# Optimization experiments

Hardware: AMD Instinct MI355X
Metric: run time of the kernel (lower is better)

The kernel has to match this reference:

```python
import jax, jax.numpy as jnp
import numpy as np

D, H, L, V, B, S, M, MAXLEN = 512, 8, 6, 32000, 16, 128, 196, 256
DK = D // H


def layernorm(x, g, b, eps):
    mu = jnp.mean(x, axis=-1, keepdims=True)
    var = jnp.mean((x - mu) ** 2, axis=-1, keepdims=True)
    return (x - mu) / jnp.sqrt(var + eps) * g + b


def mha(q_in, k_in, v_in, qw, qb, kw, kb, vw, vb, ow, ob, lng, lnb, mask):
    bs, sq = q_in.shape[0], q_in.shape[1]
    sk = k_in.shape[1]
    residual = q_in
    q = (q_in @ qw + qb).reshape(bs, sq, H, DK).transpose(0, 2, 1, 3)
    k = (k_in @ kw + kb).reshape(bs, sk, H, DK).transpose(0, 2, 1, 3)
    v = (v_in @ vw + vb).reshape(bs, sk, H, DK).transpose(0, 2, 1, 3)
    # NOTE: original divides by d_k, not sqrt(d_k)
    scores = jnp.einsum('bhqd,bhkd->bhqk', q, k) / DK
    if mask is not None:
        scores = jnp.where(mask[:, None, :, :] == 0, jnp.float32(-1e9), scores)
    attn = jax.nn.softmax(scores, axis=-1)
    o = jnp.einsum('bhqk,bhkd->bhqd', attn, v).transpose(0, 2, 1, 3).reshape(bs, sq, D)
    o = o @ ow + ob
    return layernorm(o + residual, lng, lnb, 1e-8)


def setup_inputs() -> dict:
    key = jax.random.key(0)
    ks = iter(jax.random.split(key, 64))
    std = 0.02
    inp = {}
    inp['x'] = jax.random.randint(next(ks), (B, S), 0, V, dtype=jnp.int32)
    inp['memory'] = jax.random.normal(next(ks), (B, M, D), dtype=jnp.float32)
    causal = jnp.tril(jnp.ones((S, S), dtype=jnp.int32))
    inp['mask'] = jnp.broadcast_to(causal[None], (B, S, S))
    inp['embed'] = jax.random.normal(next(ks), (V, D), dtype=jnp.float32) * std
    inp['pos'] = jax.random.uniform(next(ks), (MAXLEN, D), dtype=jnp.float32)
    for pre in ('sa', 'ca'):
        for nm in ('qw', 'kw', 'vw', 'ow'):
            inp[f'{pre}_{nm}'] = jax.random.normal(next(ks), (L, D, D), dtype=jnp.float32) * std
        for nm in ('qb', 'kb', 'vb', 'ob', 'lnb'):
            inp[f'{pre}_{nm}'] = jnp.zeros((L, D), dtype=jnp.float32)
        inp[f'{pre}_lng'] = jnp.ones((L, D), dtype=jnp.float32)
    inp['ff_w1'] = jax.random.normal(next(ks), (L, D, 4 * D), dtype=jnp.float32) * std
    inp['ff_b1'] = jnp.zeros((L, 4 * D), dtype=jnp.float32)
    inp['ff_w2'] = jax.random.normal(next(ks), (L, 4 * D, D), dtype=jnp.float32) * std
    inp['ff_b2'] = jnp.zeros((L, D), dtype=jnp.float32)
    inp['ff_lng'] = jnp.ones((L, D), dtype=jnp.float32)
    inp['ff_lnb'] = jnp.zeros((L, D), dtype=jnp.float32)
    inp['logit_w'] = jax.random.normal(next(ks), (D, V), dtype=jnp.float32) * std
    inp['logit_b'] = jnp.zeros((V,), dtype=jnp.float32)
    return inp


def reference(x, memory, mask, embed, pos,
              sa_qw, sa_qb, sa_kw, sa_kb, sa_vw, sa_vb, sa_ow, sa_ob, sa_lng, sa_lnb,
              ca_qw, ca_qb, ca_kw, ca_kb, ca_vw, ca_vb, ca_ow, ca_ob, ca_lng, ca_lnb,
              ff_w1, ff_b1, ff_w2, ff_b2, ff_lng, ff_lnb, logit_w, logit_b):
    h = embed[x] + pos[:x.shape[1], :]
    for i in range(L):
        # masked self-attention
        h = mha(h, h, h, sa_qw[i], sa_qb[i], sa_kw[i], sa_kb[i], sa_vw[i], sa_vb[i],
                sa_ow[i], sa_ob[i], sa_lng[i], sa_lnb[i], mask)
        # cross-attention over memory (no mask)
        h = mha(h, memory, memory, ca_qw[i], ca_qb[i], ca_kw[i], ca_kb[i], ca_vw[i], ca_vb[i],
                ca_ow[i], ca_ob[i], ca_lng[i], ca_lnb[i], None)
        # feed-forward (dropout is identity in eval)
        ff = jax.nn.relu(h @ ff_w1[i] + ff_b1[i]) @ ff_w2[i] + ff_b2[i]
        h = layernorm(ff + h, ff_lng[i], ff_lnb[i], 1e-6)
    return h @ logit_w + logit_b
```

## Files before the change

kernel.cpp:

```cpp
#include <hip/hip_runtime.h>
#include <cstdint>

#define D_MODEL 512
#define NHEAD   8
#define DKH     64
#define NLAYER  6
#define BATCH   16
#define SEQ     128
#define MEMS    196
#define NROWS   (BATCH*SEQ)
#define MROWS   (BATCH*MEMS)
#define SQW     (512*512)
#define SP_SELF 128
#define SP_CROSS 224

typedef __attribute__((ext_vector_type(8))) short short8;
typedef __attribute__((ext_vector_type(4))) short short4v;
typedef __attribute__((ext_vector_type(4))) float floatx4;

__device__ __forceinline__ short f2bf(float f) {
    unsigned u = __builtin_bit_cast(unsigned, f);
    u += 0x7fffu + ((u >> 16) & 1u);
    return (short)(u >> 16);
}

#define GLD16(g, l) __builtin_amdgcn_global_load_lds( \
    (const __attribute__((address_space(1))) void*)(g), \
    (__attribute__((address_space(3))) void*)(l), 16, 0, 0)

__global__ __launch_bounds__(128) void embed_kernel(
    const int* __restrict__ x, const float* __restrict__ emb,
    const float* __restrict__ pos, float* __restrict__ h, ushort* __restrict__ hb)
{
    const int row = blockIdx.x;
    const int s   = row & (SEQ - 1);
    const int tok = x[row];
    const int c   = threadIdx.x * 4;
    const float4 e = *(const float4*)(emb + (size_t)tok * D_MODEL + c);
    const float4 p = *(const float4*)(pos + (size_t)s   * D_MODEL + c);
    float4 o;
    o.x = e.x + p.x; o.y = e.y + p.y; o.z = e.z + p.z; o.w = e.w + p.w;
    *(float4*)(h + (size_t)row * D_MODEL + c) = o;
    const short4v ob = { f2bf(o.x), f2bf(o.y), f2bf(o.z), f2bf(o.w) };
    *(short4v*)(hb + (size_t)row * D_MODEL + c) = ob;
}

__device__ __forceinline__ void wtrans_tile(
    const float* __restrict__ In, ushort* __restrict__ Out,
    int K, int N, int tk, int tx)
{
    __shared__ ushort t[32][33];
    const int tid = threadIdx.x;
    const int r  = tid >> 3;
    const int c4 = (tid & 7) << 2;
    const float4 v = *(const float4*)(In + (size_t)(tk * 32 + r) * N + tx * 32 + c4);
    t[c4 + 0][r] = (ushort)f2bf(v.x);
    t[c4 + 1][r] = (ushort)f2bf(v.y);
    t[c4 + 2][r] = (ushort)f2bf(v.z);
    t[c4 + 3][r] = (ushort)f2bf(v.w);
    __syncthreads();
    const short4v o = { (short)t[r][c4], (short)t[r][c4 + 1],
                        (short)t[r][c4 + 2], (short)t[r][c4 + 3] };
    *(short4v*)(Out + (size_t)(tx * 32 + r) * K + tk * 32 + c4) = o;
}

struct Ptr8 { const float* p[8]; };

__global__ __launch_bounds__(256) void wtrans_sq(Ptr8 ps, ushort* __restrict__ out)
{
    const int mat = blockIdx.y;
    const int a = mat / 6, l = mat - a * 6;
    const float* In = ps.p[a] + (size_t)l * SQW;
    ushort* Out = out + (size_t)mat * SQW;
    const int tx = blockIdx.x & 15, tk = blockIdx.x >> 4;
    wtrans_tile(In, Out, 512, 512, tk, tx);
}

__global__ __launch_bounds__(256) void wtrans_rect(
    const float* __restrict__ in, ushort* __restrict__ out, int K, int N)
{
    const float* In = in + (size_t)blockIdx.z * K * N;
    ushort* Out = out + (size_t)blockIdx.z * K * N;
    const int ntx = N >> 5;
    const int tx = blockIdx.x % ntx, tk = blockIdx.x / ntx;
    wtrans_tile(In, Out, K, N, tk, tx);
}

__global__ __launch_bounds__(256) void convb(
    const float* __restrict__ in, ushort* __restrict__ out)
{
    const size_t i = ((size_t)blockIdx.x * 256 + threadIdx.x) * 8;
    const float4 a = *(const float4*)(in + i);
    const float4 b = *(const float4*)(in + i + 4);
    const short8 o = { f2bf(a.x), f2bf(a.y), f2bf(a.z), f2bf(a.w),
                       f2bf(b.x), f2bf(b.y), f2bf(b.z), f2bf(b.w) };
    *(short8*)(out + i) = o;
}

__global__ __launch_bounds__(256) void vtrans_kernel(
    const ushort* __restrict__ V, ushort* __restrict__ VT,
    int Sk, int SP, size_t lsV, size_t lsT)
{
    const int bh = blockIdx.x;
    const int s0 = blockIdx.y << 5;
    const int l  = blockIdx.z >> 1;
    const int d0 = (blockIdx.z & 1) << 5;
    const int b = bh >> 3, hh = bh & 7;
    const ushort* Vl = V + (size_t)l * lsV;
    ushort* Tl = VT + (size_t)l * lsT;
    __shared__ ushort t[32][36];
    const int tid = threadIdx.x;
    {
        const int sl = tid >> 3, d4 = (tid & 7) << 2;
        short4v v = {0, 0, 0, 0};
        const int s = s0 + sl;
        if (s < Sk)
            v = *(const short4v*)&Vl[(size_t)(b * Sk + s) * D_MODEL + hh * DKH + d0 + d4];
        t[sl][d4 + 0] = (ushort)v[0];
        t[sl][d4 + 1] = (ushort)v[1];
        t[sl][d4 + 2] = (ushort)v[2];
        t[sl][d4 + 3] = (ushort)v[3];
    }
    __syncthreads();
    {
        const int dl = tid >> 3, s4 = (tid & 7) << 2;
        const short4v o = { (short)t[s4 + 0][dl], (short)t[s4 + 1][dl],
                            (short)t[s4 + 2][dl], (short)t[s4 + 3][dl] };
        *(short4v*)&Tl[((size_t)(bh * 64) + d0 + dl) * SP + s0 + s4] = o;
    }
}

template<int BM, int BN>
__device__ __forceinline__ void bgemm_core(
    const ushort* __restrict__ A, const ushort* __restrict__ WT,
    const float* __restrict__ bias, float* __restrict__ Cf,
    ushort* __restrict__ Cb, int M, int K, int N, int relu)
{
    constexpr int WM = (BM >= 64) ? 2 : 1;
    constexpr int WN = 4 / WM;
    constexpr int RM = BM / (WM * 16);
    constexpr int RN = BN / (WN * 16);
    constexpr int SA = BM / 16;
    constexpr int SB = BN / 16;
    constexpr int ST = SA + SB;

    __shared__ __align__(16) ushort As[2][BM * 32];
    __shared__ __align__(16) ushort Bs[2][BN * 32];

    const int tid  = threadIdx.x;
    const int lane = tid & 63, wave = tid >> 6;
    const int m0 = blockIdx.x * BM, n0 = blockIdx.y * BN;
    const int wm = (wave % WM) * (16 * RM);
    const int wn = (wave / WM) * (16 * RN);
    const int fm = lane & 15, fq = lane >> 4;
    const int rdoff = ((fq ^ ((fm >> 2) & 3)) << 3);

    const int srow = lane >> 2;
    const int soff = (((lane & 3) ^ ((lane >> 4) & 3)) << 3);

    floatx4 acc[RM][RN] = {};

    auto stage = [&](int buf, int k0) {
        #pragma unroll
        for (int s = 0; s < ST; ++s) {
            if ((s & 3) != wave) continue;
            if (s < SA)
                GLD16(A + (size_t)(m0 + s * 16 + srow) * K + k0 + soff,
                      &As[buf][s * 512]);
            else
                GLD16(WT + (size_t)(n0 + (s - SA) * 16 + srow) * K + k0 + soff,
                      &Bs[buf][(s - SA) * 512]);
        }
    };

    stage(0, 0);
    __syncthreads();
    const int NT = K >> 5;
    int cur = 0;
    for (int t = 0; t < NT; ++t) {
        if (t + 1 < NT) stage(cur ^ 1, (t + 1) << 5);
        short8 af[RM], bfr[RN];
        #pragma unroll
        for (int i = 0; i < RM; ++i)
            af[i] = *(const short8*)&As[cur][(wm + i * 16 + fm) * 32 + rdoff];
        #pragma unroll
        for (int j = 0; j < RN; ++j)
            bfr[j] = *(const short8*)&Bs[cur][(wn + j * 16 + fm) * 32 + rdoff];
        #pragma unroll
        for (int i = 0; i < RM; ++i)
            #pragma unroll
            for (int j = 0; j < RN; ++j)
                acc[i][j] = __builtin_amdgcn_mfma_f32_16x16x32_bf16(
                                af[i], bfr[j], acc[i][j], 0, 0, 0);
        __syncthreads();
        cur ^= 1;
    }

    #pragma unroll
    for (int j = 0; j < RN; ++j) {
        const int col = n0 + wn + j * 16 + fm;
        const float bv = bias[col];
        #pragma unroll
        for (int i = 0; i < RM; ++i) {
            const int r0 = m0 + wm + i * 16 + fq * 4;
            #pragma unroll
            for (int r = 0; r < 4; ++r) {
                float v = acc[i][j][r] + bv;
                if (relu) v = fmaxf(v, 0.f);
                const size_t idx = (size_t)(r0 + r) * N + col;
                if (Cf) Cf[idx] = v;
                if (Cb) Cb[idx] = (ushort)f2bf(v);
            }
        }
    }
}

template<int BM, int BN>
__global__ __launch_bounds__(256) void bgemm(
    const ushort* __restrict__ A,
    const ushort* W0, const float* b0, float* F0, ushort* O0,
    const ushort* W1, const float* b1, float* F1, ushort* O1,
    const ushort* W2, const float* b2, float* F2, ushort* O2,
    int M, int K, int N, int relu)
{
    const ushort* W; const float* bb; float* F; ushort* Ob;
    if (blockIdx.z == 0)      { W = W0; bb = b0; F = F0; Ob = O0; }
    else if (blockIdx.z == 1) { W = W1; bb = b1; F = F1; Ob = O1; }
    else                      { W = W2; bb = b2; F = F2; Ob = O2; }
    bgemm_core<BM, BN>(A, W, bb, F, Ob, M, K, N, relu);
}

template<int BM, int BN>
__global__ __launch_bounds__(256) void bgemm_kv(
    const ushort* __restrict__ A,
    const ushort* Wk, const float* bk, ushort* Ck,
    const ushort* Wv, const float* bv, ushort* Cv,
    int M, int K, int N)
{
    const int l = blockIdx.z >> 1;
    const bool isv = blockIdx.z & 1;
    const ushort* W = (isv ? Wv : Wk) + (size_t)l * K * N;
    const float* bb = (isv ? bv : bk) + (size_t)l * N;
    ushort* C       = (isv ? Cv : Ck) + (size_t)l * M * N;
    bgemm_core<BM, BN>(A, W, bb, (float*)nullptr, C, M, K, N, 0);
}

__global__ __launch_bounds__(256) void mgemm_f32(
    const float* __restrict__ A, const float* __restrict__ W,
    const float* __restrict__ bias, float* __restrict__ C,
    int M, int K, int N, int relu)
{
    constexpr int BM = 128, BN = 128;
    constexpr int RM = BM / 32, RN = BN / 32;
    constexpr int TPR = 256 / BM;
    constexpr int ANV = BM / 32;
    constexpr int BACT = 2 * BN;

    __shared__ __align__(16) short As[BM * 32];
    __shared__ __align__(16) short Bs[BN * 32];

    const int tid = threadIdx.x;
    const int m0 = blockIdx.x * BM, n0 = blockIdx.y * BN;
    const int lane = tid & 63;
    const int wave = tid >> 6;
    const int wm = (wave >> 1) * (BM / 2), wn = (wave & 1) * (BN / 2);
    const int fm = lane & 15;
    const int fq = lane >> 4;
    const int fsw = ((fq ^ ((fm >> 2) & 3)) << 3);

    floatx4 acc[RM][RN] = {};

    const int ar = tid / TPR;
    const int ac = (tid % TPR) * (32 / TPR);
    const int asw = (ar >> 2) & 3;
    const int kb = (tid / (BN / 4)) * 4;
    const int nb = (tid % (BN / 4)) * 4;
    const int bsw = (((kb >> 3) ^ ((nb >> 2) & 3)) << 3) + (kb & 7);

    const int arow = min(m0 + ar, M - 1);
    const float* Ap = A + (size_t)arow * K + ac;
    const float* Wp = W + (size_t)kb * N + n0 + nb;

    for (int k0 = 0; k0 < K; k0 += 32) {
        float4 av[ANV];
        #pragma unroll
        for (int i = 0; i < ANV; ++i)
            av[i] = *(const float4*)(Ap + k0 + 4 * i);
        float4 w0 = {0,0,0,0}, w1 = {0,0,0,0}, w2 = {0,0,0,0}, w3 = {0,0,0,0};
        if (tid < BACT) {
            w0 = *(const float4*)(Wp + (size_t)(k0    ) * N);
            w1 = *(const float4*)(Wp + (size_t)(k0 + 1) * N);
            w2 = *(const float4*)(Wp + (size_t)(k0 + 2) * N);
            w3 = *(const float4*)(Wp + (size_t)(k0 + 3) * N);
        }
        __syncthreads();
        #pragma unroll
        for (int c = 0; c < ANV / 2; ++c) {
            const float4 lo = av[2 * c], hi = av[2 * c + 1];
            const short8 s8 = { f2bf(lo.x), f2bf(lo.y), f2bf(lo.z), f2bf(lo.w),
                                f2bf(hi.x), f2bf(hi.y), f2bf(hi.z), f2bf(hi.w) };
            *(short8*)&As[ar * 32 + ((((ac >> 3) + c) ^ asw) << 3)] = s8;
        }
        if (tid < BACT) {
            const float wt[4][4] = {{w0.x, w0.y, w0.z, w0.w},
                                    {w1.x, w1.y, w1.z, w1.w},
                                    {w2.x, w2.y, w2.z, w2.w},
                                    {w3.x, w3.y, w3.z, w3.w}};
            #pragma unroll
            for (int j = 0; j < 4; ++j) {
                const short4v bw = { f2bf(wt[0][j]), f2bf(wt[1][j]),
                                     f2bf(wt[2][j]), f2bf(wt[3][j]) };
                *(short4v*)&Bs[(nb + j) * 32 + bsw] = bw;
            }
        }
        __syncthreads();
        short8 af[RM], bfrag[RN];
        #pragma unroll
        for (int i = 0; i < RM; ++i)
            af[i] = *(const short8*)&As[(wm + i * 16 + fm) * 32 + fsw];
        #pragma unroll
        for (int j = 0; j < RN; ++j)
            bfrag[j] = *(const short8*)&Bs[(wn + j * 16 + fm) * 32 + fsw];
        #pragma unroll
        for (int i = 0; i < RM; ++i)
            #pragma unroll
            for (int j = 0; j < RN; ++j)
                acc[i][j] = __builtin_amdgcn_mfma_f32_16x16x32_bf16(
                                af[i], bfrag[j], acc[i][j], 0, 0, 0);
    }
    #pragma unroll
    for (int j = 0; j < RN; ++j) {
        const int col = n0 + wn + j * 16 + fm;
        const float bv = bias[col];
        #pragma unroll
        for (int i = 0; i < RM; ++i) {
            const int r0 = m0 + wm + i * 16 + fq * 4;
            #pragma unroll
            for (int r = 0; r < 4; ++r) {
                const int row = r0 + r;
                if (row < M) {
                    float v = acc[i][j][r] + bv;
                    if (relu) v = fmaxf(v, 0.f);
                    C[(size_t)row * N + col] = v;
                }
            }
        }
    }
}

__global__ __launch_bounds__(256) void attn_mfma(
    const ushort* __restrict__ Q, const ushort* __restrict__ K,
    const ushort* __restrict__ VT, ushort* __restrict__ O,
    int Sk, int SP, int causal)
{
    const int qt = blockIdx.x;
    const int hh = blockIdx.y;
    const int b  = blockIdx.z;
    const int tid = threadIdx.x;
    const int lane = tid & 63, wave = tid >> 6;
    const int fm = lane & 15, fq = lane >> 4;

    __shared__ __align__(16) float  Slds[16 * 225];
    __shared__ __align__(16) ushort Plds[16 * 232];
    __shared__ float invs[16];

    const int KT   = (Sk + 15) >> 4;
    const int KT16 = KT << 4;
    const int CH   = SP >> 5;

    for (int j = tid; j < 16 * 225; j += 256) Slds[j] = -1e30f;
    {
        const short8 z = {0,0,0,0,0,0,0,0};
        for (int j = tid; j < (16 * 232) / 8; j += 256) ((short8*)Plds)[j] = z;
    }
    const int q0 = qt << 4;
    const size_t qbase = ((size_t)(b * SEQ) + q0 + fm) * D_MODEL + hh * DKH;
    const short8 qf0 = *(const short8*)&Q[qbase + fq * 8];
    const short8 qf1 = *(const short8*)&Q[qbase + 32 + fq * 8];
    __syncthreads();

    const int KTeff = causal ? min(KT, qt + 1) : KT;
    for (int kt = wave; kt < KTeff; kt += 4) {
        const int krow = kt * 16 + fm;
        const size_t kbase =
            ((size_t)(b * Sk) + min(krow, Sk - 1)) * D_MODEL + hh * DKH;
        const short8 kf0 = *(const short8*)&K[kbase + fq * 8];
        const short8 kf1 = *(const short8*)&K[kbase + 32 + fq * 8];
        floatx4 s = {0.f, 0.f, 0.f, 0.f};
        s = __builtin_amdgcn_mfma_f32_16x16x32_bf16(qf0, kf0, s, 0, 0, 0);
        s = __builtin_amdgcn_mfma_f32_16x16x32_bf16(qf1, kf1, s, 0, 0, 0);
        #pragma unroll
        for (int r = 0; r < 4; ++r) {
            const int qrow = q0 + fq * 4 + r;
            const int j = kt * 16 + fm;
            const float val = (j >= Sk || (causal && j > qrow))
                              ? -1e30f : s[r] * (1.0f / 64.0f);
            Slds[(fq * 4 + r) * 225 + j] = val;
        }
    }
    __syncthreads();

    {
        const int row = tid >> 4, c = tid & 15;
        float m = -1e30f;
        for (int j = c; j < KT16; j += 16) m = fmaxf(m, Slds[row * 225 + j]);
        #pragma unroll
        for (int off = 8; off > 0; off >>= 1) m = fmaxf(m, __shfl_xor(m, off));
        float sum = 0.f;
        for (int j = c; j < KT16; j += 16) {
            const float e = __expf(Slds[row * 225 + j] - m);
            Plds[row * 232 + j] = (ushort)f2bf(e);
            sum += e;
        }
        #pragma unroll
        for (int off = 8; off > 0; off >>= 1) sum += __shfl_xor(sum, off);
        if (c == 0) invs[row] = 1.0f / sum;
    }
    __syncthreads();

    floatx4 o = {0.f, 0.f, 0.f, 0.f};
    const size_t vbase = ((size_t)(b * 8 + hh) * 64 + wave * 16 + fm) * SP;
    for (int ch = 0; ch < CH; ++ch) {
        const short8 pf = *(const short8*)&Plds[fm * 232 + ch * 32 + fq * 8];
        const short8 vf = *(const short8*)&VT[vbase + ch * 32 + fq * 8];
        o = __builtin_amdgcn_mfma_f32_16x16x32_bf16(pf, vf, o, 0, 0, 0);
    }
    #pragma unroll
    for (int r = 0; r < 4; ++r) {
        const int qrow = fq * 4 + r;
        const float val = o[r] * invs[qrow];
        O[((size_t)(b * SEQ) + q0 + qrow) * D_MODEL + hh * DKH + wave * 16 + fm]
            = (ushort)f2bf(val);
    }
}

__global__ __launch_bounds__(256) void ln_kernel(
    const float* __restrict__ X, const float* __restrict__ R,
    const float* __restrict__ g, const float* __restrict__ bb,
    float* __restrict__ Y, ushort* __restrict__ Yb, float eps)
{
    const int row = blockIdx.x;
    const int tid = threadIdx.x;
    const int lane = tid & 63, wave = tid >> 6;
    __shared__ float wred[8];
    const size_t base = (size_t)row * D_MODEL;
    const float x0 = X[base + tid]       + R[base + tid];
    const float x1 = X[base + 256 + tid] + R[base + 256 + tid];
    float sm = x0 + x1;
    #pragma unroll
    for (int off = 32; off > 0; off >>= 1) sm += __shfl_xor(sm, off);
    if (lane == 0) wred[wave] = sm;
    __syncthreads();
    const float mu = (wred[0] + wred[1] + wred[2] + wred[3]) * (1.0f / D_MODEL);
    const float d0 = x0 - mu, d1 = x1 - mu;
    float vs = d0 * d0 + d1 * d1;
    #pragma unroll
    for (int off = 32; off > 0; off >>= 1) vs += __shfl_xor(vs, off);
    if (lane == 0) wred[4 + wave] = vs;
    __syncthreads();
    const float var  = (wred[4] + wred[5] + wred[6] + wred[7]) * (1.0f / D_MODEL);
    const float rstd = rsqrtf(var + eps);
    const float y0 = d0 * rstd * g[tid]       + bb[tid];
    const float y1 = d1 * rstd * g[256 + tid] + bb[256 + tid];
    Y[base + tid]       = y0;
    Y[base + 256 + tid] = y1;
    Yb[base + tid]       = (ushort)f2bf(y0);
    Yb[base + 256 + tid] = (ushort)f2bf(y1);
}

extern "C" void kernel_launch(void* const* d_in, const int* in_sizes, int n_in,
                              void* d_out, int out_size, void* d_ws, size_t ws_size,
                              hipStream_t stream)
{
    const int*   x      = (const int*)  d_in[0];
    const float* memory = (const float*)d_in[1];
    const float* emb    = (const float*)d_in[3];
    const float* pos    = (const float*)d_in[4];
    const float* sa_qw  = (const float*)d_in[5];
    const float* sa_kw  = (const float*)d_in[6];
    const float* sa_vw  = (const float*)d_in[7];
    const float* sa_ow  = (const float*)d_in[8];
    const float* sa_qb  = (const float*)d_in[9];
    const float* sa_kb  = (const float*)d_in[10];
    const float* sa_vb  = (const float*)d_in[11];
    const float* sa_ob  = (const float*)d_in[12];
    const float* sa_lnb = (const float*)d_in[13];
    const float* sa_lng = (const float*)d_in[14];
    const float* ca_qw  = (const float*)d_in[15];
    const float* ca_kw  = (const float*)d_in[16];
    const float* ca_vw  = (const float*)d_in[17];
    const float* ca_ow  = (const float*)d_in[18];
    const float* ca_qb  = (const float*)d_in[19];
    const float* ca_kb  = (const float*)d_in[20];
    const float* ca_vb  = (const float*)d_in[21];
    const float* ca_ob  = (const float*)d_in[22];
    const float* ca_lnb = (const float*)d_in[23];
    const float* ca_lng = (const float*)d_in[24];
    const float* ff_w1  = (const float*)d_in[25];
    const float* ff_b1  = (const float*)d_in[26];
    const float* ff_w2  = (const float*)d_in[27];
    const float* ff_b2  = (const float*)d_in[28];
    const float* ff_lng = (const float*)d_in[29];
    const float* ff_lnb = (const float*)d_in[30];
    const float* logit_w= (const float*)d_in[31];
    const float* logit_b= (const float*)d_in[32];

    float* out = (float*)d_out;
    const size_t ROWB = (size_t)NROWS * D_MODEL;

    const size_t WS_H    = ROWB * 4;
    const size_t WS_HB   = ROWB * 2;
    const size_t WS_WLOG = 512ull * 32000 * 2;
    const bool wsBig = ws_size >= WS_H + WS_HB + WS_WLOG + 1024;

    char* wp = (char*)d_ws;
    float*  h     = (float*)wp;
    ushort* hb_ws = (ushort*)(wp + WS_H);
    ushort* wlogT = (ushort*)(wp + WS_H + WS_HB);

    char* op = (char*)d_out;
    auto take = [](char*& p, size_t bytes) {
        char* r = p; p += (bytes + 255) & ~(size_t)255; return r;
    };
    const size_t KVOFF  = (size_t)MROWS * D_MODEL;
    const size_t VTOFF  = (size_t)BATCH * NHEAD * DKH * SP_CROSS;
    ushort* memb  = (ushort*)take(op, (size_t)MROWS * 512 * 2);
    ushort* wsq   = (ushort*)take(op, 48ull * SQW * 2);
    ushort* w1T   = (ushort*)take(op, 6ull * 1048576 * 2);
    ushort* w2T   = (ushort*)take(op, 6ull * 1048576 * 2);
    ushort* kallb = (ushort*)take(op, 6ull * KVOFF * 2);
    ushort* vallb = (ushort*)take(op, 6ull * KVOFF * 2);
    ushort* vallT = (ushort*)take(op, 6ull * VTOFF * 2);
    ushort* qbb   = (ushort*)take(op, ROWB * 2);
    ushort* kbb   = (ushort*)take(op, ROWB * 2);
    ushort* vbb   = (ushort*)take(op, ROWB * 2);
    ushort* vbT   = (ushort*)take(op, (size_t)BATCH * NHEAD * DKH * SP_SELF * 2);
    ushort* attb  = (ushort*)take(op, ROWB * 2);
    float*  proj  = (float*)take(op, ROWB * 4);
    ushort* ffhb  = (ushort*)take(op, (size_t)NROWS * 2048 * 2);
    ushort* hb    = wsBig ? hb_ws : (ushort*)take(op, ROWB * 2);

    Ptr8 ps;
    ps.p[0] = sa_qw; ps.p[1] = sa_kw; ps.p[2] = sa_vw; ps.p[3] = sa_ow;
    ps.p[4] = ca_qw; ps.p[5] = ca_kw; ps.p[6] = ca_vw; ps.p[7] = ca_ow;
    wtrans_sq<<<dim3(256, 48), 256, 0, stream>>>(ps, wsq);
    wtrans_rect<<<dim3(1024, 1, 6), 256, 0, stream>>>(ff_w1, w1T, 512, 2048);
    wtrans_rect<<<dim3(1024, 1, 6), 256, 0, stream>>>(ff_w2, w2T, 2048, 512);
    if (wsBig)
        wtrans_rect<<<dim3(16000, 1, 1), 256, 0, stream>>>(logit_w, wlogT, 512, 32000);
    convb<<<(MROWS * 512) / 2048, 256, 0, stream>>>(memory, memb);

    embed_kernel<<<NROWS, 128, 0, stream>>>(x, emb, pos, h, hb);

    bgemm_kv<64, 64><<<dim3(MROWS / 64, 8, 2 * NLAYER), 256, 0, stream>>>(
        memb, wsq + 30ull * SQW, ca_kb, kallb,
              wsq + 36ull * SQW, ca_vb, vallb, MROWS, 512, 512);
    vtrans_kernel<<<dim3(128, SP_CROSS / 32, 2 * NLAYER), 256, 0, stream>>>(
        vallb, vallT, MEMS, SP_CROSS, KVOFF, VTOFF);

    const dim3 gattn(SEQ / 16, NHEAD, BATCH);
    const dim3 g512(NROWS / 32, 8, 1);
    const dim3 gqkv(NROWS / 64, 8, 3);

    for (int l = 0; l < NLAYER; ++l) {
        const size_t b1 = (size_t)l * D_MODEL;
        bgemm<64, 64><<<gqkv, 256, 0, stream>>>(hb,
            wsq + (size_t)(0 * 6 + l) * SQW, sa_qb + b1, nullptr, qbb,
            wsq + (size_t)(1 * 6 + l) * SQW, sa_kb + b1, nullptr, kbb,
            wsq + (size_t)(2 * 6 + l) * SQW, sa_vb + b1, nullptr, vbb,
            NROWS, 512, 512, 0);
        vtrans_kernel<<<dim3(128, SP_SELF / 32, 2), 256, 0, stream>>>(
            vbb, vbT, SEQ, SP_SELF, 0, 0);
        attn_mfma<<<gattn, 256, 0, stream>>>(qbb, kbb, vbT, attb, SEQ, SP_SELF, 1);
        bgemm<32, 64><<<g512, 256, 0, stream>>>(attb,
            wsq + (size_t)(3 * 6 + l) * SQW, sa_ob + b1, proj, nullptr,
            wsq + (size_t)(3 * 6 + l) * SQW, sa_ob + b1, proj, nullptr,
            wsq + (size_t)(3 * 6 + l) * SQW, sa_ob + b1, proj, nullptr,
            NROWS, 512, 512, 0);
        ln_kernel<<<NROWS, 256, 0, stream>>>(proj, h, sa_lng + b1, sa_lnb + b1,
                                             h, hb, 1e-8f);
        bgemm<32, 64><<<g512, 256, 0, stream>>>(hb,
            wsq + (size_t)(4 * 6 + l) * SQW, ca_qb + b1, nullptr, qbb,
            wsq + (size_t)(4 * 6 + l) * SQW, ca_qb + b1, nullptr, qbb,
            wsq + (size_t)(4 * 6 + l) * SQW, ca_qb + b1, nullptr, qbb,
            NROWS, 512, 512, 0);
        attn_mfma<<<gattn, 256, 0, stream>>>(qbb, kallb + l * KVOFF,
                                             vallT + l * VTOFF, attb,
                                             MEMS, SP_CROSS, 0);
        bgemm<32, 64><<<g512, 256, 0, stream>>>(attb,
            wsq + (size_t)(7 * 6 + l) * SQW, ca_ob + b1, proj, nullptr,
            wsq + (size_t)(7 * 6 + l) * SQW, ca_ob + b1, proj, nullptr,
            wsq + (size_t)(7 * 6 + l) * SQW, ca_ob + b1, proj, nullptr,
            NROWS, 512, 512, 0);
        ln_kernel<<<NROWS, 256, 0, stream>>>(proj, h, ca_lng + b1, ca_lnb + b1,
                                             h, hb, 1e-8f);
        bgemm<64, 64><<<dim3(NROWS / 64, 2048 / 64, 1), 256, 0, stream>>>(hb,
            w1T + (size_t)l * 1048576, ff_b1 + (size_t)l * 2048, nullptr, ffhb,
            w1T + (size_t)l * 1048576, ff_b1 + (size_t)l * 2048, nullptr, ffhb,
            w1T + (size_t)l * 1048576, ff_b1 + (size_t)l * 2048, nullptr, ffhb,
            NROWS, 512, 2048, 1);
        bgemm<32, 64><<<g512, 256, 0, stream>>>(ffhb,
            w2T + (size_t)l * 1048576, ff_b2 + b1, proj, nullptr,
            w2T + (size_t)l * 1048576, ff_b2 + b1, proj, nullptr,
            w2T + (size_t)l * 1048576, ff_b2 + b1, proj, nullptr,
            NROWS, 2048, 512, 0);
        ln_kernel<<<NROWS, 256, 0, stream>>>(proj, h, ff_lng + b1, ff_lnb + b1,
                                             h, hb, 1e-6f);
    }
    if (wsBig) {
        bgemm<128, 128><<<dim3(NROWS / 128, 32000 / 128, 1), 256, 0, stream>>>(hb,
            wlogT, logit_b, out, nullptr,
            wlogT, logit_b, out, nullptr,
            wlogT, logit_b, out, nullptr, NROWS, 512, 32000, 0);
    } else {
        mgemm_f32<<<dim3(NROWS / 128, 32000 / 128, 1), 256, 0, stream>>>(
            h, logit_w, logit_b, out, NROWS, 512, 32000, 0);
    }
}
```

Measured before the change: 1.445 ms.

## Double bgemm K-tile to 64 and add weight-stationary logit GEMM kernel

Measured after the change: 1.536 ms. 6.3% more time.

```diff
diff --git a/kernel.cpp b/kernel.cpp
--- a/kernel.cpp
+++ b/kernel.cpp
@@ -140,12 +140,12 @@
     constexpr int WN = 4 / WM;
     constexpr int RM = BM / (WM * 16);
     constexpr int RN = BN / (WN * 16);
-    constexpr int SA = BM / 16;
-    constexpr int SB = BN / 16;
+    constexpr int SA = (BM / 16) * 2;
+    constexpr int SB = (BN / 16) * 2;
     constexpr int ST = SA + SB;
 
-    __shared__ __align__(16) ushort As[2][BM * 32];
-    __shared__ __align__(16) ushort Bs[2][BN * 32];
+    __shared__ __align__(16) ushort As[2][BM * 64];
+    __shared__ __align__(16) ushort Bs[2][BN * 64];
 
     const int tid  = threadIdx.x;
     const int lane = tid & 63, wave = tid >> 6;
@@ -164,34 +164,42 @@
         #pragma unroll
         for (int s = 0; s < ST; ++s) {
             if ((s & 3) != wave) continue;
-            if (s < SA)
-                GLD16(A + (size_t)(m0 + s * 16 + srow) * K + k0 + soff,
+            if (s < SA) {
+                const int rg = s >> 1, kc = s & 1;
+                GLD16(A + (size_t)(m0 + rg * 16 + srow) * K + k0 + kc * 32 + soff,
                       &As[buf][s * 512]);
-            else
-                GLD16(WT + (size_t)(n0 + (s - SA) * 16 + srow) * K + k0 + soff,
-                      &Bs[buf][(s - SA) * 512]);
+            } else {
+                const int s2 = s - SA, rg = s2 >> 1, kc = s2 & 1;
+                GLD16(WT + (size_t)(n0 + rg * 16 + srow) * K + k0 + kc * 32 + soff,
+                      &Bs[buf][s2 * 512]);
+            }
         }
     };
 
     stage(0, 0);
     __syncthreads();
-    const int NT = K >> 5;
+    const int NT = K >> 6;
     int cur = 0;
     for (int t = 0; t < NT; ++t) {
-        if (t + 1 < NT) stage(cur ^ 1, (t + 1) << 5);
-        short8 af[RM], bfr[RN];
-        #pragma unroll
-        for (int i = 0; i < RM; ++i)
-            af[i] = *(const short8*)&As[cur][(wm + i * 16 + fm) * 32 + rdoff];
-        #pragma unroll
-        for (int j = 0; j < RN; ++j)
-            bfr[j] = *(const short8*)&Bs[cur][(wn + j * 16 + fm) * 32 + rdoff];
-        #pragma unroll
-        for (int i = 0; i < RM; ++i)
+        if (t + 1 < NT) stage(cur ^ 1, (t + 1) << 6);
+        #pragma unroll
+        for (int kc = 0; kc < 2; ++kc) {
+            short8 af[RM], bfr[RN];
+            #pragma unroll
+            for (int i = 0; i < RM; ++i)
+                af[i] = *(const short8*)
+                    &As[cur][((wm / 16 + i) * 2 + kc) * 512 + fm * 32 + rdoff];
             #pragma unroll
             for (int j = 0; j < RN; ++j)
-                acc[i][j] = __builtin_amdgcn_mfma_f32_16x16x32_bf16(
-                                af[i], bfr[j], acc[i][j], 0, 0, 0);
+                bfr[j] = *(const short8*)
+                    &Bs[cur][((wn / 16 + j) * 2 + kc) * 512 + fm * 32 + rdoff];
+            #pragma unroll
+            for (int i = 0; i < RM; ++i)
+                #pragma unroll
+                for (int j = 0; j < RN; ++j)
+                    acc[i][j] = __builtin_amdgcn_mfma_f32_16x16x32_bf16(
+                                    af[i], bfr[j], acc[i][j], 0, 0, 0);
+        }
         __syncthreads();
         cur ^= 1;
     }
@@ -243,6 +251,70 @@
     const float* bb = (isv ? bv : bk) + (size_t)l * N;
     ushort* C       = (isv ? Cv : Ck) + (size_t)l * M * N;
     bgemm_core<BM, BN>(A, W, bb, (float*)nullptr, C, M, K, N, 0);
+}
+
+__global__ __launch_bounds__(256) void logit_gemm(
+    const ushort* __restrict__ A, const ushort* __restrict__ WT,
+    const float* __restrict__ bias, float* __restrict__ C)
+{
+    __shared__ __align__(16) ushort Ws[64 * 512];
+    const int tid = threadIdx.x;
+    const int lane = tid & 63, wave = tid >> 6;
+    const int n0 = blockIdx.x << 6;
+    const int fm = lane & 15, fq = lane >> 4;
+    const int rdoff = ((fq ^ ((fm >> 2) & 3)) << 3);
+    const int srow = lane >> 2;
+    const int soff = (((lane & 3) ^ ((lane >> 4) & 3)) << 3);
+
+    #pragma unroll
+    for (int s = 0; s < 64; ++s) {
+        if ((s & 3) != wave) continue;
+        const int rg = s >> 4, kc = s & 15;
+        GLD16(WT + (size_t)(n0 + rg * 16 + srow) * 512 + kc * 32 + soff,
+              &Ws[s * 512]);
+    }
+    __syncthreads();
+
+    const int wm = (wave & 1) << 6;
+    const int wn = (wave >> 1) << 5;
+    float bv[2];
+    #pragma unroll
+    for (int j = 0; j < 2; ++j) bv[j] = bias[n0 + wn + j * 16 + fm];
+
+    for (int mt = 0; mt < 16; ++mt) {
+        const int m0 = mt << 7;
+        floatx4 acc[4][2] = {};
+        #pragma unroll
+        for (int kc = 0; kc < 16; ++kc) {
+            short8 af[4], bf2[2];
+            #pragma unroll
+            for (int i = 0; i < 4; ++i)
+                af[i] = *(const short8*)
+                    &A[(size_t)(m0 + wm + i * 16 + fm) * 512 + kc * 32 + fq * 8];
+            #pragma unroll
+            for (int j = 0; j < 2; ++j) {
+                const int rg = (wn >> 4) + j;
+                bf2[j] = *(const short8*)&Ws[(rg * 16 + kc) * 512 + fm * 32 + rdoff];
+            }
+            #pragma unroll
+            for (int i = 0; i < 4; ++i)
+                #pragma unroll
+                for (int j = 0; j < 2; ++j)
+                    acc[i][j] = __builtin_amdgcn_mfma_f32_16x16x32_bf16(
+                                    af[i], bf2[j], acc[i][j], 0, 0, 0);
+        }
+        #pragma unroll
+        for (int j = 0; j < 2; ++j) {
+            const int col = n0 + wn + j * 16 + fm;
+            #pragma unroll
+            for (int i = 0; i < 4; ++i) {
+                const int r0 = m0 + wm + i * 16 + fq * 4;
+                #pragma unroll
+                for (int r = 0; r < 4; ++r)
+                    C[(size_t)(r0 + r) * 32000 + col] = acc[i][j][r] + bv[j];
+            }
+        }
+    }
 }
 
 __global__ __launch_bounds__(256) void mgemm_f32(
@@ -608,10 +680,7 @@
                                              h, hb, 1e-6f);
     }
     if (wsBig) {
-        bgemm<128, 128><<<dim3(NROWS / 128, 32000 / 128, 1), 256, 0, stream>>>(hb,
-            wlogT, logit_b, out, nullptr,
-            wlogT, logit_b, out, nullptr,
-            wlogT, logit_b, out, nullptr, NROWS, 512, 32000, 0);
+        logit_gemm<<<500, 256, 0, stream>>>(hb, wlogT, logit_b, out);
     } else {
         mgemm_f32<<<dim3(NROWS / 128, 32000 / 128, 1), 256, 0, stream>>>(
             h, logit_w, logit_b, out, NROWS, 512, 32000, 0);
```
